# Performance work log

Measured on AMD Instinct MI355X. Metric: run time of the kernel, lower is better.

## Reference

```python
import jax, jax.numpy as jnp
import numpy as np

C = 256
HEADS = 4
GROUPS = 8
EPS = 1e-5


def setup_inputs() -> dict:
    key = jax.random.key(0)
    ks = jax.random.split(key, 7)
    B, H, W = 2, 64, 64
    x = jax.random.normal(ks[0], (B, C, H, W), dtype=jnp.float32)
    gamma = jnp.ones((C,), dtype=jnp.float32)
    beta = jnp.zeros((C,), dtype=jnp.float32)
    # conv 1x1 weights stored as [out_ch, in_ch]
    w_qkv = jax.random.normal(ks[1], (3 * C, C), dtype=jnp.float32) * (1.0 / np.sqrt(C))
    b_qkv = jax.random.normal(ks[2], (3 * C,), dtype=jnp.float32) * 0.01
    w_proj = jax.random.normal(ks[3], (C, C), dtype=jnp.float32) * (1.0 / np.sqrt(C))
    b_proj = jax.random.normal(ks[4], (C,), dtype=jnp.float32) * 0.01
    return {"x": x, "gamma": gamma, "beta": beta, "w_qkv": w_qkv,
            "b_qkv": b_qkv, "w_proj": w_proj, "b_proj": b_proj}


def _group_norm(x, gamma, beta):
    B, Cc, H, W = x.shape
    xg = x.reshape(B, GROUPS, Cc // GROUPS, H, W)
    mean = xg.mean(axis=(2, 3, 4), keepdims=True)
    var = xg.var(axis=(2, 3, 4), keepdims=True)
    xg = (xg - mean) * jax.lax.rsqrt(var + EPS)
    xn = xg.reshape(B, Cc, H, W)
    return xn * gamma[None, :, None, None] + beta[None, :, None, None]


def reference(x, gamma, beta, w_qkv, b_qkv, w_proj, b_proj):
    B, Cc, H, W = x.shape
    N = H * W
    hd = Cc // HEADS
    residual = x
    xn = _group_norm(x, gamma, beta)
    # 1x1 conv == channel matmul: [B,3C,H,W]
    qkv = jnp.einsum('oc,bchw->bohw', w_qkv, xn) + b_qkv[None, :, None, None]
    # [B,3,heads,hd,N] -> (3,B,heads,N,hd)
    qkv = qkv.reshape(B, 3, HEADS, hd, N).transpose(1, 0, 2, 4, 3)
    q, k, v = qkv[0], qkv[1], qkv[2]
    scale = hd ** -0.5
    attn = jax.nn.softmax(jnp.einsum('bhnd,bhmd->bhnm', q, k) * scale, axis=-1)
    out = jnp.einsum('bhnm,bhmd->bhnd', attn, v)  # [B,heads,N,hd]
    out = out.transpose(0, 1, 3, 2).reshape(B, Cc, H, W)
    out = jnp.einsum('oc,bchw->bohw', w_proj, out) + b_proj[None, :, None, None]
    return out + residual
```

## Files before the change

### kernel.cpp

```cpp
#include <hip/hip_runtime.h>
#include <stdint.h>

#define EPS 1e-5f

typedef float f32x4 __attribute__((ext_vector_type(4)));
typedef float f32x16 __attribute__((ext_vector_type(16)));
typedef __bf16 bf16x8 __attribute__((ext_vector_type(8)));
typedef uint32_t u32x4 __attribute__((ext_vector_type(4)));

__device__ __forceinline__ ushort f2bf(float f){
  union { float f; uint32_t u; } v; v.f = f;
  uint32_t r = v.u + 0x7fffu + ((v.u >> 16) & 1u);
  return (ushort)(r >> 16);
}

__device__ __forceinline__ float bf2f(ushort u){
  union { uint32_t u; float f; } v; v.u = ((uint32_t)u) << 16;
  return v.f;
}

__device__ __forceinline__ uint32_t pk2bf(float a, float b){
  __bf16 x = (__bf16)a, y = (__bf16)b;
  return (uint32_t)__builtin_bit_cast(ushort, x) |
         ((uint32_t)__builtin_bit_cast(ushort, y) << 16);
}

__device__ __forceinline__ f32x4 mfma16(bf16x8 a, bf16x8 b, f32x4 c){
  return __builtin_amdgcn_mfma_f32_16x16x32_bf16(a, b, c, 0, 0, 0);
}
__device__ __forceinline__ f32x16 mfma32(bf16x8 a, bf16x8 b, f32x16 c){
  return __builtin_amdgcn_mfma_f32_32x32x16_bf16(a, b, c, 0, 0, 0);
}

__global__ __launch_bounds__(256) void k_pg(const float* wq, const float* wp, const float* x,
                                            ushort* wqb, ushort* wpb, float2* part){
  __shared__ float red[8];
  int bid = blockIdx.x;
  if (bid < 768){
    int i = bid * 256 + threadIdx.x;
    if (i < 3*256*256) wqb[i] = f2bf(wq[i]);
    if (i < 256*256)   wpb[i] = f2bf(wp[i]);
    return;
  }
  int gb = bid - 768;
  int bg = gb >> 6, pb = gb & 63;
  const f32x4* base = (const f32x4*)(x + (size_t)bg*131072 + (size_t)pb*2048);
  float s = 0.f, ss = 0.f;
  #pragma unroll
  for (int it = 0; it < 2; ++it){
    f32x4 v = base[threadIdx.x + it*256];
    #pragma unroll
    for (int j = 0; j < 4; ++j){ s += v[j]; ss += v[j]*v[j]; }
  }
  #pragma unroll
  for (int off = 1; off < 64; off <<= 1){
    s  += __shfl_xor(s,  off);
    ss += __shfl_xor(ss, off);
  }
  int wid = threadIdx.x >> 6;
  if ((threadIdx.x & 63) == 0){ red[wid] = s; red[4 + wid] = ss; }
  __syncthreads();
  if (threadIdx.x == 0){
    part[gb] = make_float2(red[0]+red[1]+red[2]+red[3],
                           red[4]+red[5]+red[6]+red[7]);
  }
}

__global__ __launch_bounds__(512) void k_nqkv(const float* x, const float* gamma, const float* beta,
                                              const float2* part, const ushort* wqb, const float* bqkv,
                                              ushort* Qf, ushort* Kf, ushort* Vf){
  __shared__ ushort A[32][264];
  __shared__ ushort Cl[32][136];
  __shared__ ushort Cl_T[128][40];
  __shared__ float2 st[8];
  const float SCL2 = 0.125f * 1.44269504f;
  int nt = blockIdx.x, b = blockIdx.y;
  int t = threadIdx.x, lane = t & 63, wid = t >> 6;

  {
    float2 p = part[(b*8 + wid)*64 + lane];
    float s = p.x, ss = p.y;
    #pragma unroll
    for (int off = 1; off < 64; off <<= 1){
      s  += __shfl_xor(s,  off);
      ss += __shfl_xor(ss, off);
    }
    if (lane == 0){
      const float inv = 1.f / 131072.f;
      float mean = s * inv;
      float var  = ss * inv - mean*mean;
      st[wid] = make_float2(mean, rsqrtf(var + EPS));
    }
  }
  __syncthreads();

  {
    int c = t >> 1, nh = t & 1;
    float2 s0 = st[c >> 5];
    float g  = gamma[c] * s0.y;
    float bt = beta[c] - s0.x * g;
    const float* xr = x + ((size_t)(b*256 + c))*4096 + nt*32 + nh*16;
    #pragma unroll
    for (int j4 = 0; j4 < 4; ++j4){
      f32x4 v = *(const f32x4*)(xr + j4*4);
      #pragma unroll
      for (int e = 0; e < 4; ++e) A[nh*16 + j4*4 + e][c] = f2bf(v[e]*g + bt);
    }
  }
  __syncthreads();

  int l15 = lane & 15, g4 = lane >> 4;
  f32x4 acc[6][2];
  #pragma unroll
  for (int of = 0; of < 6; ++of)
    #pragma unroll
    for (int mf = 0; mf < 2; ++mf) acc[of][mf] = (f32x4){0.f,0.f,0.f,0.f};

  #pragma unroll
  for (int ks = 0; ks < 8; ++ks){
    bf16x8 a0 = *(const bf16x8*)&A[l15][ks*32 + g4*8];
    bf16x8 a1 = *(const bf16x8*)&A[16 + l15][ks*32 + g4*8];
    #pragma unroll
    for (int of = 0; of < 6; ++of){
      int o = of*128 + wid*16 + l15;
      bf16x8 bw = *(const bf16x8*)(wqb + (size_t)o*256 + ks*32 + g4*8);
      acc[of][0] = mfma16(a0, bw, acc[of][0]);
      acc[of][1] = mfma16(a1, bw, acc[of][1]);
    }
  }

  #pragma unroll
  for (int of = 0; of < 6; ++of){
    __syncthreads();
    float bias = bqkv[of*128 + wid*16 + l15];
    if (of < 4){
      float scl = (of < 2) ? SCL2 : 1.f;
      #pragma unroll
      for (int mf = 0; mf < 2; ++mf)
        #pragma unroll
        for (int r = 0; r < 4; ++r)
          Cl[mf*16 + g4*4 + r][wid*16 + l15] = f2bf((acc[of][mf][r] + bias) * scl);
    } else {
      #pragma unroll
      for (int mf = 0; mf < 2; ++mf)
        *(uint2*)&Cl_T[wid*16 + l15][mf*16 + g4*4] =
          make_uint2(pk2bf(acc[of][mf][0]+bias, acc[of][mf][1]+bias),
                     pk2bf(acc[of][mf][2]+bias, acc[of][mf][3]+bias));
    }
    __syncthreads();

    int hp = t >> 8;
    int hh = (of & 1)*2 + hp;
    if (of < 4){
      int rem = t & 255, dsub = rem >> 6, ln = rem & 63, h2 = ln >> 5, p31 = ln & 31;
      int row = (of < 2) ? p31 : ((p31 & 19) | ((p31 & 4) << 1) | ((p31 & 8) >> 1));
      ushort* basep = (of < 2) ? Qf : Kf;
      uint4 v = *(const uint4*)&Cl[row][hp*64 + dsub*16 + h2*8];
      *(uint4*)(basep + ((size_t)(b*4 + hh))*262144 + nt*2048 + dsub*512 + ln*8) = v;
    } else {
      int rem = t & 255, dt = rem >> 7, r2 = rem & 127, c4h = r2 >> 5, p31 = r2 & 31;
      int c4 = (nt & 1)*2 + (c4h >> 1), h2 = c4h & 1;
      int n0 = (c4h >> 1)*16 + h2*8;
      int ln = h2*32 + p31;
      uint4 v = *(const uint4*)&Cl_T[hp*64 + dt*32 + p31][n0];
      *(uint4*)(Vf + ((size_t)(b*4 + hh))*262144 + (size_t)(nt >> 1)*4096
                   + dt*2048 + c4*512 + ln*8) = v;
    }
  }
}

template<int SPLIT>
__global__ __launch_bounds__(256, 3) void k_attn(const ushort* Qf, const ushort* Kf,
                                                 const ushort* Vf, ushort* Opart, float2* ML){
  int bh = blockIdx.x & 7;
  int within = blockIdx.x >> 3;
  int sp = within >> 5, qg = within & 31;
  int t = threadIdx.x, wid = t >> 6, l = t & 63, l31 = l & 31, hi = l >> 5;
  int qt = qg*4 + wid;

  const ushort* Qg = Qf + (size_t)bh*262144 + qt*2048 + l*8;
  const ushort* Kg = Kf + (size_t)bh*262144 + l*8;
  const ushort* Vg = Vf + (size_t)bh*262144 + l*8;

  bf16x8 qf[4];
  #pragma unroll
  for (int dsub = 0; dsub < 4; ++dsub)
    qf[dsub] = *(const bf16x8*)(Qg + dsub*512);

  f32x16 o[2];
  #pragma unroll
  for (int dt = 0; dt < 2; ++dt)
    #pragma unroll
    for (int r = 0; r < 16; ++r) o[dt][r] = 0.f;
  float m_s = -INFINITY, l_s = 0.f;

  const int kbBeg = sp * (64 / SPLIT), kbEnd = kbBeg + 64 / SPLIT;
  for (int kb = kbBeg; kb < kbEnd; ++kb){
    bf16x8 kf[2][4];
    #pragma unroll
    for (int kt = 0; kt < 2; ++kt)
      #pragma unroll
      for (int dsub = 0; dsub < 4; ++dsub)
        kf[kt][dsub] = *(const bf16x8*)(Kg + (size_t)(kb*2 + kt)*2048 + dsub*512);

    bf16x8 vf[2][4];
    #pragma unroll
    for (int dt = 0; dt < 2; ++dt)
      #pragma unroll
      for (int c4 = 0; c4 < 4; ++c4)
        vf[dt][c4] = *(const bf16x8*)(Vg + (size_t)kb*4096 + dt*2048 + c4*512);

    f32x16 s[2];
    __builtin_amdgcn_s_setprio(1);
    #pragma unroll
    for (int kt = 0; kt < 2; ++kt){
      f32x16 acc;
      #pragma unroll
      for (int r = 0; r < 16; ++r) acc[r] = 0.f;
      #pragma unroll
      for (int dsub = 0; dsub < 4; ++dsub)
        acc = mfma32(kf[kt][dsub], qf[dsub], acc);
      s[kt] = acc;
    }
    __builtin_amdgcn_s_setprio(0);

    f32x16 mx = s[0];
    #pragma unroll
    for (int r = 0; r < 16; ++r) mx[r] = fmaxf(mx[r], s[1][r]);
    #pragma unroll
    for (int off = 8; off > 0; off >>= 1)
      #pragma unroll
      for (int r = 0; r < off; ++r) mx[r] = fmaxf(mx[r], mx[r + off]);
    float vm = fmaxf(mx[0], __shfl_xor(mx[0], 32));

    if (__any(vm > m_s + 8.f)){
      float mn = fmaxf(m_s, vm);
      float a = __builtin_amdgcn_exp2f(m_s - mn);
      m_s = mn; l_s *= a;
      #pragma unroll
      for (int dt = 0; dt < 2; ++dt)
        #pragma unroll
        for (int r = 0; r < 16; ++r) o[dt][r] *= a;
    }
    {
      float r0 = 0.f, r1 = 0.f, r2 = 0.f, r3 = 0.f;
      #pragma unroll
      for (int kt = 0; kt < 2; ++kt)
        #pragma unroll
        for (int r = 0; r < 16; r += 4){
          float e0 = __builtin_amdgcn_exp2f(s[kt][r+0] - m_s);
          float e1 = __builtin_amdgcn_exp2f(s[kt][r+1] - m_s);
          float e2 = __builtin_amdgcn_exp2f(s[kt][r+2] - m_s);
          float e3 = __builtin_amdgcn_exp2f(s[kt][r+3] - m_s);
          s[kt][r+0] = e0; s[kt][r+1] = e1;
          s[kt][r+2] = e2; s[kt][r+3] = e3;
          r0 += e0; r1 += e1; r2 += e2; r3 += e3;
        }
      float rr = (r0 + r1) + (r2 + r3);
      rr += __shfl_xor(rr, 32);
      l_s += rr;
    }

    bf16x8 pf[2][2];
    #pragma unroll
    for (int kt = 0; kt < 2; ++kt)
      #pragma unroll
      for (int ks = 0; ks < 2; ++ks){
        u32x4 w;
        #pragma unroll
        for (int c = 0; c < 4; ++c)
          w[c] = pk2bf(s[kt][8*ks + 2*c], s[kt][8*ks + 2*c + 1]);
        pf[kt][ks] = __builtin_bit_cast(bf16x8, w);
      }

    __builtin_amdgcn_s_setprio(1);
    #pragma unroll
    for (int dt = 0; dt < 2; ++dt)
      #pragma unroll
      for (int kt = 0; kt < 2; ++kt)
        #pragma unroll
        for (int ks = 0; ks < 2; ++ks)
          o[dt] = mfma32(vf[dt][kt*2 + ks], pf[kt][ks], o[dt]);
    __builtin_amdgcn_s_setprio(0);
  }

  int pw = (bh*SPLIT + sp)*128 + qt;
  if (hi == 0) ML[(size_t)pw*32 + l31] = make_float2(m_s, l_s);
  ushort* dst = Opart + (size_t)pw*2048;
  #pragma unroll
  for (int dt = 0; dt < 2; ++dt)
    #pragma unroll
    for (int rq = 0; rq < 4; ++rq){
      int d0 = dt*32 + rq*8 + 4*hi;
      uint2 w = make_uint2(pk2bf(o[dt][rq*4+0], o[dt][rq*4+1]),
                           pk2bf(o[dt][rq*4+2], o[dt][rq*4+3]));
      *(uint2*)(dst + (size_t)l31*64 + d0) = w;
    }
}

template<int SPLIT>
__global__ __launch_bounds__(256) void k_cproj(const ushort* Opart, const float2* ML,
                                               const ushort* wpb, const float* bproj,
                                               const float* x, float* out){
  __shared__ ushort A[32][264];
  int nt = blockIdx.x, b = blockIdx.y;
  int t = threadIdx.x;

  int n_local = t >> 3, d0 = (t & 7) * 8;
  #pragma unroll
  for (int h = 0; h < 4; ++h){
    int bh = b*4 + h;
    float2 mls[SPLIT];
    float m = -INFINITY;
    #pragma unroll
    for (int sp = 0; sp < SPLIT; ++sp){
      mls[sp] = ML[((size_t)((bh*SPLIT + sp)*128 + nt))*32 + n_local];
      m = fmaxf(m, mls[sp].x);
    }
    float den = 0.f, w[SPLIT];
    #pragma unroll
    for (int sp = 0; sp < SPLIT; ++sp){
      w[sp] = __builtin_amdgcn_exp2f(mls[sp].x - m);
      den += mls[sp].y * w[sp];
    }
    float inv = 1.f / den;
    float vals[8];
    #pragma unroll
    for (int j = 0; j < 8; ++j) vals[j] = 0.f;
    #pragma unroll
    for (int sp = 0; sp < SPLIT; ++sp){
      const ushort* src = Opart + ((size_t)((bh*SPLIT + sp)*128 + nt))*2048 + (size_t)n_local*64 + d0;
      uint4 a0 = *(const uint4*)src;
      float f = w[sp] * inv;
      #pragma unroll
      for (int j = 0; j < 8; ++j) vals[j] += bf2f(((const ushort*)&a0)[j]) * f;
    }
    uint32_t pk[4];
    #pragma unroll
    for (int j = 0; j < 4; ++j) pk[j] = pk2bf(vals[2*j], vals[2*j+1]);
    *(uint4*)&A[n_local][h*64 + d0] = make_uint4(pk[0], pk[1], pk[2], pk[3]);
  }
  __syncthreads();

  int lane = t & 63, wid = t >> 6, l15 = lane & 15, g4 = lane >> 4;
  f32x4 acc[4][2];
  #pragma unroll
  for (int of = 0; of < 4; ++of)
    #pragma unroll
    for (int mf = 0; mf < 2; ++mf) acc[of][mf] = (f32x4){0.f,0.f,0.f,0.f};

  #pragma unroll
  for (int ks = 0; ks < 8; ++ks){
    bf16x8 aa0 = *(const bf16x8*)&A[l15][ks*32 + g4*8];
    bf16x8 aa1 = *(const bf16x8*)&A[16 + l15][ks*32 + g4*8];
    #pragma unroll
    for (int of = 0; of < 4; ++of){
      int o = wid*64 + of*16 + l15;
      bf16x8 bw = *(const bf16x8*)(wpb + (size_t)o*256 + ks*32 + g4*8);
      acc[of][0] = mfma16(aa0, bw, acc[of][0]);
      acc[of][1] = mfma16(aa1, bw, acc[of][1]);
    }
  }

  #pragma unroll
  for (int of = 0; of < 4; ++of){
    int o = wid*64 + of*16 + l15;
    float bias = bproj[o];
    size_t cbase = ((size_t)b*256 + o)*4096;
    #pragma unroll
    for (int mf = 0; mf < 2; ++mf){
      int n0 = nt*32 + mf*16 + g4*4;
      f32x4 res = *(const f32x4*)(x + cbase + n0);
      f32x4 ov;
      #pragma unroll
      for (int r = 0; r < 4; ++r) ov[r] = acc[of][mf][r] + bias + res[r];
      *(f32x4*)(out + cbase + n0) = ov;
    }
  }
}

extern "C" void kernel_launch(void* const* d_in, const int* in_sizes, int n_in,
                              void* d_out, int out_size, void* d_ws, size_t ws_size,
                              hipStream_t stream) {
  const float* x     = (const float*)d_in[0];
  const float* gamma = (const float*)d_in[1];
  const float* beta  = (const float*)d_in[2];
  const float* wqkv  = (const float*)d_in[3];
  const float* bqkv  = (const float*)d_in[4];
  const float* wproj = (const float*)d_in[5];
  const float* bproj = (const float*)d_in[6];
  float* out = (float*)d_out;

  const size_t MiB = 1024*1024;
  char* ws = (char*)d_ws;
  float2* part   = (float2*)(ws + 0);
  ushort* wq_b   = (ushort*)(ws + 16384);
  ushort* wp_b   = (ushort*)(ws + 409600);
  ushort* Qf     = (ushort*)(ws + 1*MiB);
  ushort* Kf     = (ushort*)(ws + 5*MiB);
  ushort* Vf     = (ushort*)(ws + 9*MiB);
  ushort* Opart  = (ushort*)(ws + 13*MiB);

  int split = (ws_size >= 31*MiB) ? 4 : 2;
  float2* ML = (float2*)(ws + (13 + 4*(size_t)split)*MiB);

  k_pg  <<<1792, 256, 0, stream>>>(wqkv, wproj, x, wq_b, wp_b, part);
  k_nqkv<<<dim3(128,2), 512, 0, stream>>>(x, gamma, beta, part, wq_b, bqkv, Qf, Kf, Vf);
  if (split == 4){
    k_attn<4><<<1024, 256, 0, stream>>>(Qf, Kf, Vf, Opart, ML);
    k_cproj<4><<<dim3(128,2), 256, 0, stream>>>(Opart, ML, wp_b, bproj, x, out);
  } else {
    k_attn<2><<<512, 256, 0, stream>>>(Qf, Kf, Vf, Opart, ML);
    k_cproj<2><<<dim3(128,2), 256, 0, stream>>>(Opart, ML, wp_b, bproj, x, out);
  }
}
```

Measured before the change: 154.4 us.

## Split norm and QKV kernels, stage K/V through LDS, widen proj blocks

Splits the fused norm+QKV kernel into a separate normalization kernel that writes a bf16 normalized token-major buffer, plus a QKV GEMM kernel gridded over Q/K/V type, which raises block count from 256 to 768. The attention kernel now cooperatively loads K/V tiles into double-buffered shared memory with a register prefetch of the next tile. Previously each wave loaded them directly from global memory. The combine+projection kernel uses 512 threads with fewer output tiles per wave. This trades an extra launch and an extra round trip through global memory for the normalized activations against more parallelism and shared K/V reuse across the four waves of a block.

```diff
diff --git a/kernel.cpp b/kernel.cpp
--- a/kernel.cpp
+++ b/kernel.cpp
@@ -66,26 +66,22 @@
   }
 }
 
-__global__ __launch_bounds__(512) void k_nqkv(const float* x, const float* gamma, const float* beta,
-                                              const float2* part, const ushort* wqb, const float* bqkv,
-                                              ushort* Qf, ushort* Kf, ushort* Vf){
-  __shared__ ushort A[32][264];
-  __shared__ ushort Cl[32][136];
-  __shared__ ushort Cl_T[128][40];
-  __shared__ float2 st[8];
-  const float SCL2 = 0.125f * 1.44269504f;
-  int nt = blockIdx.x, b = blockIdx.y;
-  int t = threadIdx.x, lane = t & 63, wid = t >> 6;
-
-  {
-    float2 p = part[(b*8 + wid)*64 + lane];
+__global__ __launch_bounds__(256) void k_norm(const float* x, const float* gamma, const float* beta,
+                                              const float2* part, ushort* Xn){
+  __shared__ float T[64][65];
+  __shared__ float2 st[2];
+  int nt = blockIdx.x, ct = blockIdx.y, b = blockIdx.z;
+  int t = threadIdx.x, wid = t >> 6, ln = t & 63;
+
+  if (wid < 2){
+    float2 p = part[((b*8) + ct*2 + wid)*64 + ln];
     float s = p.x, ss = p.y;
     #pragma unroll
     for (int off = 1; off < 64; off <<= 1){
       s  += __shfl_xor(s,  off);
       ss += __shfl_xor(ss, off);
     }
-    if (lane == 0){
+    if (ln == 0){
       const float inv = 1.f / 131072.f;
       float mean = s * inv;
       float var  = ss * inv - mean*mean;
@@ -94,77 +90,101 @@
   }
   __syncthreads();
 
-  {
-    int c = t >> 1, nh = t & 1;
-    float2 s0 = st[c >> 5];
-    float g  = gamma[c] * s0.y;
-    float bt = beta[c] - s0.x * g;
-    const float* xr = x + ((size_t)(b*256 + c))*4096 + nt*32 + nh*16;
-    #pragma unroll
-    for (int j4 = 0; j4 < 4; ++j4){
-      f32x4 v = *(const f32x4*)(xr + j4*4);
-      #pragma unroll
-      for (int e = 0; e < 4; ++e) A[nh*16 + j4*4 + e][c] = f2bf(v[e]*g + bt);
-    }
+  int c_local = t >> 2, col0 = (t & 3) * 16;
+  float2 s0 = st[c_local >> 5];
+  float g  = gamma[ct*64 + c_local] * s0.y;
+  float bt = beta[ct*64 + c_local] - s0.x * g;
+  const float* xr = x + ((size_t)(b*256 + ct*64 + c_local))*4096 + nt*64 + col0;
+  #pragma unroll
+  for (int j = 0; j < 4; ++j){
+    f32x4 v = *(const f32x4*)(xr + j*4);
+    #pragma unroll
+    for (int e = 0; e < 4; ++e) T[col0 + j*4 + e][c_local] = v[e]*g + bt;
   }
   __syncthreads();
 
-  int l15 = lane & 15, g4 = lane >> 4;
-  f32x4 acc[6][2];
-  #pragma unroll
-  for (int of = 0; of < 6; ++of)
+  int n_local = t >> 2, c0 = (t & 3) * 16;
+  uint32_t pk[8];
+  #pragma unroll
+  for (int j = 0; j < 8; ++j) pk[j] = pk2bf(T[n_local][c0 + 2*j], T[n_local][c0 + 2*j + 1]);
+  ushort* dst = Xn + ((size_t)b*4096 + nt*64 + n_local)*256 + ct*64 + c0;
+  *(uint4*)dst       = make_uint4(pk[0], pk[1], pk[2], pk[3]);
+  *(uint4*)(dst + 8) = make_uint4(pk[4], pk[5], pk[6], pk[7]);
+}
+
+__global__ __launch_bounds__(256) void k_qkv(const ushort* Xn, const ushort* wqb, const float* bqkv,
+                                             ushort* Qf, ushort* Kf, ushort* Vf){
+  __shared__ ushort SB[10240];
+  const float SCL2 = 0.125f * 1.44269504f;
+  int nt = blockIdx.x, typ = blockIdx.y, b = blockIdx.z;
+  int t = threadIdx.x, lane = t & 63, wid = t >> 6, l15 = lane & 15, g4 = lane >> 4;
+
+  f32x4 acc[4][2];
+  #pragma unroll
+  for (int of = 0; of < 4; ++of)
     #pragma unroll
     for (int mf = 0; mf < 2; ++mf) acc[of][mf] = (f32x4){0.f,0.f,0.f,0.f};
 
+  const ushort* Ab = Xn + ((size_t)b*4096 + nt*32)*256;
   #pragma unroll
   for (int ks = 0; ks < 8; ++ks){
-    bf16x8 a0 = *(const bf16x8*)&A[l15][ks*32 + g4*8];
-    bf16x8 a1 = *(const bf16x8*)&A[16 + l15][ks*32 + g4*8];
-    #pragma unroll
-    for (int of = 0; of < 6; ++of){
-      int o = of*128 + wid*16 + l15;
-      bf16x8 bw = *(const bf16x8*)(wqb + (size_t)o*256 + ks*32 + g4*8);
-      acc[of][0] = mfma16(a0, bw, acc[of][0]);
-      acc[of][1] = mfma16(a1, bw, acc[of][1]);
-    }
-  }
-
-  #pragma unroll
-  for (int of = 0; of < 6; ++of){
-    __syncthreads();
-    float bias = bqkv[of*128 + wid*16 + l15];
-    if (of < 4){
-      float scl = (of < 2) ? SCL2 : 1.f;
+    bf16x8 aa0 = *(const bf16x8*)(Ab + (size_t)l15*256 + ks*32 + g4*8);
+    bf16x8 aa1 = *(const bf16x8*)(Ab + (size_t)(16 + l15)*256 + ks*32 + g4*8);
+    #pragma unroll
+    for (int of = 0; of < 4; ++of){
+      int ol = wid*64 + of*16 + l15;
+      bf16x8 bw = *(const bf16x8*)(wqb + ((size_t)typ*256 + ol)*256 + ks*32 + g4*8);
+      acc[of][0] = mfma16(aa0, bw, acc[of][0]);
+      acc[of][1] = mfma16(aa1, bw, acc[of][1]);
+    }
+  }
+
+  if (typ < 2){
+    ushort (*Cl)[264] = (ushort(*)[264])SB;
+    float scl = (typ == 0) ? SCL2 : 1.f;
+    #pragma unroll
+    for (int of = 0; of < 4; ++of){
+      int ol = wid*64 + of*16 + l15;
+      float bias = bqkv[typ*256 + ol];
       #pragma unroll
       for (int mf = 0; mf < 2; ++mf)
         #pragma unroll
         for (int r = 0; r < 4; ++r)
-          Cl[mf*16 + g4*4 + r][wid*16 + l15] = f2bf((acc[of][mf][r] + bias) * scl);
-    } else {
-      #pragma unroll
-      for (int mf = 0; mf < 2; ++mf)
-        *(uint2*)&Cl_T[wid*16 + l15][mf*16 + g4*4] =
-          make_uint2(pk2bf(acc[of][mf][0]+bias, acc[of][mf][1]+bias),
-                     pk2bf(acc[of][mf][2]+bias, acc[of][mf][3]+bias));
+          Cl[mf*16 + g4*4 + r][ol] = f2bf((acc[of][mf][r] + bias) * scl);
     }
     __syncthreads();
-
-    int hp = t >> 8;
-    int hh = (of & 1)*2 + hp;
-    if (of < 4){
-      int rem = t & 255, dsub = rem >> 6, ln = rem & 63, h2 = ln >> 5, p31 = ln & 31;
-      int row = (of < 2) ? p31 : ((p31 & 19) | ((p31 & 4) << 1) | ((p31 & 8) >> 1));
-      ushort* basep = (of < 2) ? Qf : Kf;
-      uint4 v = *(const uint4*)&Cl[row][hp*64 + dsub*16 + h2*8];
-      *(uint4*)(basep + ((size_t)(b*4 + hh))*262144 + nt*2048 + dsub*512 + ln*8) = v;
-    } else {
-      int rem = t & 255, dt = rem >> 7, r2 = rem & 127, c4h = r2 >> 5, p31 = r2 & 31;
-      int c4 = (nt & 1)*2 + (c4h >> 1), h2 = c4h & 1;
-      int n0 = (c4h >> 1)*16 + h2*8;
-      int ln = h2*32 + p31;
-      uint4 v = *(const uint4*)&Cl_T[hp*64 + dt*32 + p31][n0];
-      *(uint4*)(Vf + ((size_t)(b*4 + hh))*262144 + (size_t)(nt >> 1)*4096
-                   + dt*2048 + c4*512 + ln*8) = v;
+    ushort* basep = (typ == 0) ? Qf : Kf;
+    #pragma unroll
+    for (int j = 0; j < 4; ++j){
+      int u = t + j*256;
+      int h = u >> 8, r = u & 255, dsub = r >> 6, ln = r & 63, h2 = ln >> 5, p31 = ln & 31;
+      int row = (typ == 0) ? p31 : ((p31 & 19) | ((p31 & 4) << 1) | ((p31 & 8) >> 1));
+      uint4 v = *(const uint4*)&Cl[row][h*64 + dsub*16 + h2*8];
+      *(uint4*)(basep + ((size_t)(b*4 + h))*262144 + nt*2048 + dsub*512 + ln*8) = v;
+    }
+  } else {
+    ushort (*Cl_T)[40] = (ushort(*)[40])SB;
+    #pragma unroll
+    for (int of = 0; of < 4; ++of){
+      int ol = wid*64 + of*16 + l15;
+      float bias = bqkv[512 + ol];
+      #pragma unroll
+      for (int mf = 0; mf < 2; ++mf){
+        uint2 w2 = make_uint2(pk2bf(acc[of][mf][0]+bias, acc[of][mf][1]+bias),
+                              pk2bf(acc[of][mf][2]+bias, acc[of][mf][3]+bias));
+        *(uint2*)&Cl_T[ol][mf*16 + g4*4] = w2;
+      }
+    }
+    __syncthreads();
+    #pragma unroll
+    for (int j = 0; j < 4; ++j){
+      int u = t + j*256;
+      int h = u >> 8, r = u & 255, dt = r >> 7, r2 = r & 127;
+      int c4h = r2 >> 5, p31 = r2 & 31, h2 = c4h & 1, c4loc = c4h >> 1;
+      int ln = h2*32 + p31, n0 = c4loc*16 + h2*8;
+      uint4 v = *(const uint4*)&Cl_T[h*64 + dt*32 + p31][n0];
+      *(uint4*)(Vf + ((size_t)(b*4 + h))*262144 + (size_t)(nt >> 1)*4096
+                   + dt*2048 + ((nt & 1)*2 + c4loc)*512 + ln*8) = v;
     }
   }
 }
@@ -172,15 +192,17 @@
 template<int SPLIT>
 __global__ __launch_bounds__(256, 3) void k_attn(const ushort* Qf, const ushort* Kf,
                                                  const ushort* Vf, ushort* Opart, float2* ML){
+  __shared__ ushort Kl[2][4096];
+  __shared__ ushort Vl[2][4096];
   int bh = blockIdx.x & 7;
   int within = blockIdx.x >> 3;
-  int sp = within >> 5, qg = within & 31;
+  int sp = within >> 5, qb = within & 31;
   int t = threadIdx.x, wid = t >> 6, l = t & 63, l31 = l & 31, hi = l >> 5;
-  int qt = qg*4 + wid;
+  int qt = qb*4 + wid;
 
   const ushort* Qg = Qf + (size_t)bh*262144 + qt*2048 + l*8;
-  const ushort* Kg = Kf + (size_t)bh*262144 + l*8;
-  const ushort* Vg = Vf + (size_t)bh*262144 + l*8;
+  const ushort* Kt = Kf + (size_t)bh*262144;
+  const ushort* Vt = Vf + (size_t)bh*262144;
 
   bf16x8 qf[4];
   #pragma unroll
@@ -194,21 +216,33 @@
     for (int r = 0; r < 16; ++r) o[dt][r] = 0.f;
   float m_s = -INFINITY, l_s = 0.f;
 
-  const int kbBeg = sp * (64 / SPLIT), kbEnd = kbBeg + 64 / SPLIT;
-  for (int kb = kbBeg; kb < kbEnd; ++kb){
-    bf16x8 kf[2][4];
-    #pragma unroll
-    for (int kt = 0; kt < 2; ++kt)
-      #pragma unroll
-      for (int dsub = 0; dsub < 4; ++dsub)
-        kf[kt][dsub] = *(const bf16x8*)(Kg + (size_t)(kb*2 + kt)*2048 + dsub*512);
-
-    bf16x8 vf[2][4];
-    #pragma unroll
-    for (int dt = 0; dt < 2; ++dt)
-      #pragma unroll
-      for (int c4 = 0; c4 < 4; ++c4)
-        vf[dt][c4] = *(const bf16x8*)(Vg + (size_t)kb*4096 + dt*2048 + c4*512);
+  const int nIt = 64 / SPLIT;
+  const int kb0 = sp * nIt;
+
+  {
+    const ushort* Ks = Kt + (size_t)kb0*4096;
+    const ushort* Vs = Vt + (size_t)kb0*4096;
+    uint4 a0 = *(const uint4*)(Ks + t*8);
+    uint4 a1 = *(const uint4*)(Ks + 2048 + t*8);
+    uint4 a2 = *(const uint4*)(Vs + t*8);
+    uint4 a3 = *(const uint4*)(Vs + 2048 + t*8);
+    *(uint4*)&Kl[0][t*8] = a0; *(uint4*)&Kl[0][2048 + t*8] = a1;
+    *(uint4*)&Vl[0][t*8] = a2; *(uint4*)&Vl[0][2048 + t*8] = a3;
+  }
+  __syncthreads();
+
+  for (int it = 0; it < nIt; ++it){
+    int cur = it & 1;
+    bool more = (it + 1 < nIt);
+    uint4 sk0, sk1, sv0, sv1;
+    if (more){
+      const ushort* Ks = Kt + (size_t)(kb0 + it + 1)*4096;
+      const ushort* Vs = Vt + (size_t)(kb0 + it + 1)*4096;
+      sk0 = *(const uint4*)(Ks + t*8);
+      sk1 = *(const uint4*)(Ks + 2048 + t*8);
+      sv0 = *(const uint4*)(Vs + t*8);
+      sv1 = *(const uint4*)(Vs + 2048 + t*8);
+    }
 
     f32x16 s[2];
     __builtin_amdgcn_s_setprio(1);
@@ -218,8 +252,10 @@
       #pragma unroll
       for (int r = 0; r < 16; ++r) acc[r] = 0.f;
       #pragma unroll
-      for (int dsub = 0; dsub < 4; ++dsub)
-        acc = mfma32(kf[kt][dsub], qf[dsub], acc);
+      for (int dsub = 0; dsub < 4; ++dsub){
+        bf16x8 kf = *(const bf16x8*)&Kl[cur][(kt*4 + dsub)*512 + l*8];
+        acc = mfma32(kf, qf[dsub], acc);
+      }
       s[kt] = acc;
     }
     __builtin_amdgcn_s_setprio(0);
@@ -279,9 +315,17 @@
       #pragma unroll
       for (int kt = 0; kt < 2; ++kt)
         #pragma unroll
-        for (int ks = 0; ks < 2; ++ks)
-          o[dt] = mfma32(vf[dt][kt*2 + ks], pf[kt][ks], o[dt]);
+        for (int ks = 0; ks < 2; ++ks){
+          bf16x8 vf = *(const bf16x8*)&Vl[cur][(dt*4 + kt*2 + ks)*512 + l*8];
+          o[dt] = mfma32(vf, pf[kt][ks], o[dt]);
+        }
     __builtin_amdgcn_s_setprio(0);
+
+    if (more){
+      *(uint4*)&Kl[cur^1][t*8] = sk0; *(uint4*)&Kl[cur^1][2048 + t*8] = sk1;
+      *(uint4*)&Vl[cur^1][t*8] = sv0; *(uint4*)&Vl[cur^1][2048 + t*8] = sv1;
+    }
+    __syncthreads();
   }
 
   int pw = (bh*SPLIT + sp)*128 + qt;
@@ -299,16 +343,16 @@
 }
 
 template<int SPLIT>
-__global__ __launch_bounds__(256) void k_cproj(const ushort* Opart, const float2* ML,
+__global__ __launch_bounds__(512) void k_cproj(const ushort* Opart, const float2* ML,
                                                const ushort* wpb, const float* bproj,
                                                const float* x, float* out){
   __shared__ ushort A[32][264];
   int nt = blockIdx.x, b = blockIdx.y;
   int t = threadIdx.x;
 
-  int n_local = t >> 3, d0 = (t & 7) * 8;
-  #pragma unroll
-  for (int h = 0; h < 4; ++h){
+  {
+    int n_local = t >> 4, dpos = (t & 15) * 16;
+    int h = dpos >> 6, dd = dpos & 63;
     int bh = b*4 + h;
     float2 mls[SPLIT];
     float m = -INFINITY;
@@ -324,28 +368,32 @@
       den += mls[sp].y * w[sp];
     }
     float inv = 1.f / den;
-    float vals[8];
-    #pragma unroll
-    for (int j = 0; j < 8; ++j) vals[j] = 0.f;
+    float vals[16];
+    #pragma unroll
+    for (int j = 0; j < 16; ++j) vals[j] = 0.f;
     #pragma unroll
     for (int sp = 0; sp < SPLIT; ++sp){
-      const ushort* src = Opart + ((size_t)((bh*SPLIT + sp)*128 + nt))*2048 + (size_t)n_local*64 + d0;
+      const ushort* src = Opart + ((size_t)((bh*SPLIT + sp)*128 + nt))*2048 + (size_t)n_local*64 + dd;
       uint4 a0 = *(const uint4*)src;
+      uint4 a1 = *(const uint4*)(src + 8);
       float f = w[sp] * inv;
       #pragma unroll
-      for (int j = 0; j < 8; ++j) vals[j] += bf2f(((const ushort*)&a0)[j]) * f;
-    }
-    uint32_t pk[4];
-    #pragma unroll
-    for (int j = 0; j < 4; ++j) pk[j] = pk2bf(vals[2*j], vals[2*j+1]);
-    *(uint4*)&A[n_local][h*64 + d0] = make_uint4(pk[0], pk[1], pk[2], pk[3]);
+      for (int j = 0; j < 8; ++j) vals[j]     += bf2f(((const ushort*)&a0)[j]) * f;
+      #pragma unroll
+      for (int j = 0; j < 8; ++j) vals[j + 8] += bf2f(((const ushort*)&a1)[j]) * f;
+    }
+    uint32_t pk[8];
+    #pragma unroll
+    for (int j = 0; j < 8; ++j) pk[j] = pk2bf(vals[2*j], vals[2*j+1]);
+    *(uint4*)&A[n_local][dpos]     = make_uint4(pk[0], pk[1], pk[2], pk[3]);
+    *(uint4*)&A[n_local][dpos + 8] = make_uint4(pk[4], pk[5], pk[6], pk[7]);
   }
   __syncthreads();
 
   int lane = t & 63, wid = t >> 6, l15 = lane & 15, g4 = lane >> 4;
-  f32x4 acc[4][2];
-  #pragma unroll
-  for (int of = 0; of < 4; ++of)
+  f32x4 acc[2][2];
+  #pragma unroll
+  for (int of = 0; of < 2; ++of)
     #pragma unroll
     for (int mf = 0; mf < 2; ++mf) acc[of][mf] = (f32x4){0.f,0.f,0.f,0.f};
 
@@ -354,8 +402,8 @@
     bf16x8 aa0 = *(const bf16x8*)&A[l15][ks*32 + g4*8];
     bf16x8 aa1 = *(const bf16x8*)&A[16 + l15][ks*32 + g4*8];
     #pragma unroll
-    for (int of = 0; of < 4; ++of){
-      int o = wid*64 + of*16 + l15;
+    for (int of = 0; of < 2; ++of){
+      int o = wid*32 + of*16 + l15;
       bf16x8 bw = *(const bf16x8*)(wpb + (size_t)o*256 + ks*32 + g4*8);
       acc[of][0] = mfma16(aa0, bw, acc[of][0]);
       acc[of][1] = mfma16(aa1, bw, acc[of][1]);
@@ -363,8 +411,8 @@
   }
 
   #pragma unroll
-  for (int of = 0; of < 4; ++of){
-    int o = wid*64 + of*16 + l15;
+  for (int of = 0; of < 2; ++of){
+    int o = wid*32 + of*16 + l15;
     float bias = bproj[o];
     size_t cbase = ((size_t)b*256 + o)*4096;
     #pragma unroll
@@ -399,18 +447,20 @@
   ushort* Qf     = (ushort*)(ws + 1*MiB);
   ushort* Kf     = (ushort*)(ws + 5*MiB);
   ushort* Vf     = (ushort*)(ws + 9*MiB);
+  ushort* Xn     = (ushort*)(ws + 13*MiB);
   ushort* Opart  = (ushort*)(ws + 13*MiB);
 
   int split = (ws_size >= 31*MiB) ? 4 : 2;
   float2* ML = (float2*)(ws + (13 + 4*(size_t)split)*MiB);
 
   k_pg  <<<1792, 256, 0, stream>>>(wqkv, wproj, x, wq_b, wp_b, part);
-  k_nqkv<<<dim3(128,2), 512, 0, stream>>>(x, gamma, beta, part, wq_b, bqkv, Qf, Kf, Vf);
+  k_norm<<<dim3(64,4,2), 256, 0, stream>>>(x, gamma, beta, part, Xn);
+  k_qkv <<<dim3(128,3,2), 256, 0, stream>>>(Xn, wq_b, bqkv, Qf, Kf, Vf);
   if (split == 4){
     k_attn<4><<<1024, 256, 0, stream>>>(Qf, Kf, Vf, Opart, ML);
-    k_cproj<4><<<dim3(128,2), 256, 0, stream>>>(Opart, ML, wp_b, bproj, x, out);
+    k_cproj<4><<<dim3(128,2), 512, 0, stream>>>(Opart, ML, wp_b, bproj, x, out);
   } else {
     k_attn<2><<<512, 256, 0, stream>>>(Qf, Kf, Vf, Opart, ML);
-    k_cproj<2><<<dim3(128,2), 256, 0, stream>>>(Opart, ML, wp_b, bproj, x, out);
-  }
-}
+    k_cproj<2><<<dim3(128,2), 512, 0, stream>>>(Opart, ML, wp_b, bproj, x, out);
+  }
+}
```

Measured after the change: 153.6 us. About the same (-0.5%).
